# Kernel optimization log

Hardware: AMD Instinct MI355X
Metric: run time of the kernel (lower is better)

Reference implementation:

```python
import jax, jax.numpy as jnp
import numpy as np

B, T, D, H = 2, 2048, 1024, 16  # batch, seq, n_embed, n_head


def setup_inputs() -> dict:
    key = jax.random.key(0)
    ks = jax.random.split(key, 5)
    scale = 1.0 / np.sqrt(D)
    return {
        "x": jax.random.normal(ks[0], (B, T, D), dtype=jnp.float32),
        "Wq": jax.random.normal(ks[1], (D, D), dtype=jnp.float32) * scale,
        "Wk": jax.random.normal(ks[2], (D, D), dtype=jnp.float32) * scale,
        "Wv": jax.random.normal(ks[3], (D, D), dtype=jnp.float32) * scale,
        "Wo": jax.random.normal(ks[4], (D, D), dtype=jnp.float32) * scale,
    }


def reference(x, Wq, Wk, Wv, Wo):
    b, t, d = x.shape
    hd = d // H  # head_dim
    # projections -> [B, H, T, hd]
    q = (x @ Wq).reshape(b, t, H, hd).transpose(0, 2, 1, 3)
    k = (x @ Wk).reshape(b, t, H, hd).transpose(0, 2, 1, 3)
    v = (x @ Wv).reshape(b, t, H, hd).transpose(0, 2, 1, 3)
    # scaled scores [B, H, T, T] with causal mask
    e = jnp.einsum("bhqd,bhkd->bhqk", q, k) * (1.0 / np.sqrt(hd))
    causal = jnp.tril(jnp.ones((t, t), dtype=bool))
    e = jnp.where(causal[None, None], e, jnp.finfo(e.dtype).min)
    alpha = jax.nn.softmax(e, axis=-1)
    # attention output -> [B, T, D]
    attn = jnp.einsum("bhqk,bhkd->bhqd", alpha, v)
    attn = attn.transpose(0, 2, 1, 3).reshape(b, t, d)
    return attn @ Wo
```

## Files before the change

### kernel.cpp

```cpp
#include <hip/hip_runtime.h>
#include <hip/hip_bf16.h>
#include <math.h>


#define Bsz  2
#define Tseq 2048
#define Dm   1024
#define NH   16
#define HD   64

typedef short bf16x8 __attribute__((ext_vector_type(8)));
typedef float floatx4 __attribute__((ext_vector_type(4)));

__device__ __forceinline__ unsigned short f2bf(float f) {
    __hip_bfloat16 h = __float2bfloat16(f);
    return *reinterpret_cast<unsigned short*>(&h);
}

__device__ __forceinline__ unsigned short f2bf_fast(float f) {
    unsigned int u = __builtin_bit_cast(unsigned int, f);
    return (unsigned short)((u + 0x8000u) >> 16);
}

__device__ __forceinline__ void lds16(unsigned short* lds, const unsigned short* g) {
    __builtin_amdgcn_global_load_lds(
        (const __attribute__((address_space(1))) void*)g,
        (__attribute__((address_space(3))) void*)lds, 16, 0, 0);
}

__global__ __launch_bounds__(256) void cast_x(const float* __restrict__ x,
                                              unsigned short* __restrict__ xb) {
    const size_t i = (size_t)blockIdx.x * 256 + threadIdx.x;
    const float4 v = ((const float4*)x)[i];
    ushort4 o;
    o.x = f2bf(v.x); o.y = f2bf(v.y); o.z = f2bf(v.z); o.w = f2bf(v.w);
    ((ushort4*)xb)[i] = o;
}

__global__ __launch_bounds__(256) void wtrans(const float* __restrict__ W0,
                                              const float* __restrict__ W1,
                                              const float* __restrict__ W2,
                                              const float* __restrict__ W3,
                                              unsigned short* __restrict__ T0,
                                              unsigned short* __restrict__ T1,
                                              unsigned short* __restrict__ T2,
                                              unsigned short* __restrict__ T3) {
    const int z = blockIdx.z;
    const float* W = (z == 0) ? W0 : (z == 1) ? W1 : (z == 2) ? W2 : W3;
    unsigned short* T = (z == 0) ? T0 : (z == 1) ? T1 : (z == 2) ? T2 : T3;
    __shared__ float t[64][65];
    const int k0 = blockIdx.y * 64, n0 = blockIdx.x * 64;
    const int row = threadIdx.x >> 6, col = threadIdx.x & 63;
#pragma unroll
    for (int p = 0; p < 16; ++p)
        t[p * 4 + row][col] = W[(size_t)(k0 + p * 4 + row) * Dm + n0 + col];
    __syncthreads();
#pragma unroll
    for (int p = 0; p < 16; ++p)
        T[(size_t)(n0 + p * 4 + row) * Dm + k0 + col] = f2bf(t[col][p * 4 + row]);
}

__device__ __forceinline__ void gemm128_mainloop(const unsigned short* __restrict__ A,
                                                 const unsigned short* __restrict__ Bt,
                                                 int K, int m0, int n0,
                                                 unsigned short* As, unsigned short* Bs,
                                                 floatx4 acc[4][4]) {
    const int tid = threadIdx.x;
    const int lane = tid & 63, wave = tid >> 6;
    const int l15 = lane & 15, quad = lane >> 4;
    const int wm = (wave >> 1) * 64, wn = (wave & 1) * 64;

    for (int k0 = 0; k0 < K; k0 += 32) {
        __syncthreads();
#pragma unroll
        for (int c = 0; c < 2; ++c) {
            const int idx = c * 256 + tid;
            const int row = idx >> 2, kc = (idx & 3) * 8;
            lds16(&As[row * 32 + kc], A + (size_t)(m0 + row) * K + k0 + kc);
            lds16(&Bs[row * 32 + kc], Bt + (size_t)(n0 + row) * K + k0 + kc);
        }
        __syncthreads();
        bf16x8 af[4], bf[4];
#pragma unroll
        for (int i = 0; i < 4; ++i)
            af[i] = *(const bf16x8*)&As[(wm + i * 16 + l15) * 32 + quad * 8];
#pragma unroll
        for (int j = 0; j < 4; ++j)
            bf[j] = *(const bf16x8*)&Bs[(wn + j * 16 + l15) * 32 + quad * 8];
#pragma unroll
        for (int i = 0; i < 4; ++i)
#pragma unroll
            for (int j = 0; j < 4; ++j)
                acc[i][j] = __builtin_amdgcn_mfma_f32_16x16x32_bf16(af[i], bf[j], acc[i][j], 0, 0, 0);
    }
}

__global__ __launch_bounds__(256) void gemm_qkv(const unsigned short* __restrict__ xb,
                                                const unsigned short* __restrict__ Wqt,
                                                const unsigned short* __restrict__ Wkt,
                                                const unsigned short* __restrict__ Wvt,
                                                unsigned short* __restrict__ Qb,
                                                unsigned short* __restrict__ Kb,
                                                unsigned short* __restrict__ Vb) {
    __shared__ unsigned short As[128 * 32];
    __shared__ unsigned short Bs[128 * 32];
    const int z = blockIdx.z;
    const unsigned short* Bt = (z == 0) ? Wqt : (z == 1) ? Wkt : Wvt;
    unsigned short* C = (z == 0) ? Qb : (z == 1) ? Kb : Vb;
    const float scale = (z == 0) ? (0.125f * 1.4426950408889634f) : 1.0f;
    const int m0 = blockIdx.y * 128, n0 = blockIdx.x * 128;

    floatx4 acc[4][4];
#pragma unroll
    for (int i = 0; i < 4; ++i)
#pragma unroll
        for (int j = 0; j < 4; ++j) acc[i][j] = (floatx4){0.f, 0.f, 0.f, 0.f};

    gemm128_mainloop(xb, Bt, Dm, m0, n0, As, Bs, acc);

    const int lane = threadIdx.x & 63, wave = threadIdx.x >> 6;
    const int l15 = lane & 15, quad = lane >> 4;
    const int wm = (wave >> 1) * 64, wn = (wave & 1) * 64;
#pragma unroll
    for (int i = 0; i < 4; ++i)
#pragma unroll
        for (int j = 0; j < 4; ++j)
#pragma unroll
            for (int r = 0; r < 4; ++r) {
                const int row = m0 + wm + i * 16 + quad * 4 + r;
                const int col = n0 + wn + j * 16 + l15;
                C[(size_t)row * Dm + col] = f2bf(acc[i][j][r] * scale);
            }
}

__global__ __launch_bounds__(256) void gemm_out(const unsigned short* __restrict__ Yb,
                                                const unsigned short* __restrict__ Wot,
                                                float* __restrict__ out) {
    __shared__ unsigned short As[128 * 32];
    __shared__ unsigned short Bs[128 * 32];
    const int m0 = blockIdx.y * 128, n0 = blockIdx.x * 128;

    floatx4 acc[4][4];
#pragma unroll
    for (int i = 0; i < 4; ++i)
#pragma unroll
        for (int j = 0; j < 4; ++j) acc[i][j] = (floatx4){0.f, 0.f, 0.f, 0.f};

    gemm128_mainloop(Yb, Wot, Dm, m0, n0, As, Bs, acc);

    const int lane = threadIdx.x & 63, wave = threadIdx.x >> 6;
    const int l15 = lane & 15, quad = lane >> 4;
    const int wm = (wave >> 1) * 64, wn = (wave & 1) * 64;
#pragma unroll
    for (int i = 0; i < 4; ++i)
#pragma unroll
        for (int j = 0; j < 4; ++j)
#pragma unroll
            for (int r = 0; r < 4; ++r) {
                const int row = m0 + wm + i * 16 + quad * 4 + r;
                const int col = n0 + wn + j * 16 + l15;
                out[(size_t)row * Dm + col] = acc[i][j][r];
            }
}

__global__ __launch_bounds__(256) void vtrans_b(const unsigned short* __restrict__ Vb,
                                                unsigned short* __restrict__ VbT) {
    __shared__ unsigned short tile[64][72];
    const int tt = blockIdx.x;
    const int h = blockIdx.y;
    const int row = threadIdx.x >> 6, col = threadIdx.x & 63;
#pragma unroll
    for (int p = 0; p < 16; ++p)
        tile[p * 4 + row][col] = Vb[(size_t)(tt * 64 + p * 4 + row) * Dm + h * HD + col];
    __syncthreads();
    const int gt0 = tt * 64;
    const int b = gt0 / Tseq;
    const int lt0 = gt0 - b * Tseq;
#pragma unroll
    for (int p = 0; p < 16; ++p) {
        const int d = p * 4 + row;
        VbT[((size_t)(b * NH + h) * HD + d) * Tseq + lt0 + col] = tile[col][d];
    }
}

__global__ __launch_bounds__(256) void attn_mfma(const unsigned short* __restrict__ Qb,
                                                 const unsigned short* __restrict__ Kb,
                                                 const unsigned short* __restrict__ VbT,
                                                 unsigned short* __restrict__ Yb) {
    const int bh = blockIdx.x;
    const int b = bh >> 4;
    const int h = bh & 15;
    const int qt = 31 - blockIdx.y;
    const int tid = threadIdx.x;
    const int wave = tid >> 6;
    const int lane = tid & 63;
    const int l15 = lane & 15;
    const int quad = lane >> 4;

    __shared__ unsigned short Ks0[64][32];
    __shared__ unsigned short Ks1[64][32];
    __shared__ unsigned short Vt0[64][32];
    __shared__ unsigned short Vt1[64][32];
    __shared__ unsigned short Ps[4][16][72];

    const size_t tok0 = (size_t)b * Tseq;
    const int colh = h * HD;
    const unsigned short* vbase = VbT + (size_t)bh * HD * Tseq;

    const int qrow = qt * 64 + wave * 16;

    const unsigned short* qptr = Qb + (tok0 + qrow + l15) * Dm + colh + quad * 8;
    const bf16x8 qf0 = *(const bf16x8*)(qptr);
    const bf16x8 qf1 = *(const bf16x8*)(qptr + 32);

    float l_lane[4] = {0.f, 0.f, 0.f, 0.f};
    floatx4 o_acc[4];
#pragma unroll
    for (int t = 0; t < 4; ++t) o_acc[t] = (floatx4){0.f, 0.f, 0.f, 0.f};

    const int srow = tid >> 2;
    const int sc8 = (tid & 3) * 8;

    for (int kt = 0; kt <= qt; ++kt) {
        const int k0 = kt * 64;
        __syncthreads();
        {
            const unsigned short* krow = Kb + (tok0 + k0 + srow) * Dm + colh;
            const unsigned short* vrow = vbase + (size_t)srow * Tseq + k0;
            lds16(&Ks0[srow][sc8], krow + sc8);
            lds16(&Ks1[srow][sc8], krow + 32 + sc8);
            lds16(&Vt0[srow][sc8], vrow + sc8);
            lds16(&Vt1[srow][sc8], vrow + 32 + sc8);
        }
        __syncthreads();

        floatx4 s[4];
#pragma unroll
        for (int t = 0; t < 4; ++t) {
            floatx4 c = (floatx4){0.f, 0.f, 0.f, 0.f};
            const bf16x8 b0 = *(const bf16x8*)&Ks0[t * 16 + l15][quad * 8];
            const bf16x8 b1 = *(const bf16x8*)&Ks1[t * 16 + l15][quad * 8];
            c = __builtin_amdgcn_mfma_f32_16x16x32_bf16(qf0, b0, c, 0, 0, 0);
            c = __builtin_amdgcn_mfma_f32_16x16x32_bf16(qf1, b1, c, 0, 0, 0);
            s[t] = c;
        }

        if (kt == qt) {
#pragma unroll
            for (int t = 0; t < 4; ++t)
#pragma unroll
                for (int r = 0; r < 4; ++r) {
                    const int kl = t * 16 + l15;
                    const int ql = wave * 16 + quad * 4 + r;
                    if (kl > ql) s[t][r] = -1.0e30f;
                }
        }

#pragma unroll
        for (int t = 0; t < 4; ++t)
#pragma unroll
            for (int r = 0; r < 4; ++r) {
                const float p = __builtin_amdgcn_exp2f(s[t][r]);
                l_lane[r] += p;
                Ps[wave][quad * 4 + r][t * 16 + l15] = f2bf_fast(p);
            }

        const bf16x8 pa0 = *(const bf16x8*)&Ps[wave][l15][quad * 8];
        const bf16x8 pa1 = *(const bf16x8*)&Ps[wave][l15][32 + quad * 8];
#pragma unroll
        for (int t = 0; t < 4; ++t) {
            const bf16x8 vb0 = *(const bf16x8*)&Vt0[t * 16 + l15][quad * 8];
            const bf16x8 vb1 = *(const bf16x8*)&Vt1[t * 16 + l15][quad * 8];
            o_acc[t] = __builtin_amdgcn_mfma_f32_16x16x32_bf16(pa0, vb0, o_acc[t], 0, 0, 0);
            o_acc[t] = __builtin_amdgcn_mfma_f32_16x16x32_bf16(pa1, vb1, o_acc[t], 0, 0, 0);
        }
    }

#pragma unroll
    for (int off = 1; off < 16; off <<= 1)
#pragma unroll
        for (int r = 0; r < 4; ++r)
            l_lane[r] += __shfl_xor(l_lane[r], off);
    float inv_l[4];
#pragma unroll
    for (int r = 0; r < 4; ++r) inv_l[r] = 1.0f / l_lane[r];
#pragma unroll
    for (int t = 0; t < 4; ++t)
#pragma unroll
        for (int r = 0; r < 4; ++r) {
            const int q = qrow + quad * 4 + r;
            Yb[(tok0 + q) * Dm + colh + t * 16 + l15] = f2bf(o_acc[t][r] * inv_l[r]);
        }
}

extern "C" void kernel_launch(void* const* d_in, const int* in_sizes, int n_in,
                              void* d_out, int out_size, void* d_ws, size_t ws_size,
                              hipStream_t stream) {
    const float* x  = (const float*)d_in[0];
    const float* Wq = (const float*)d_in[1];
    const float* Wk = (const float*)d_in[2];
    const float* Wv = (const float*)d_in[3];
    const float* Wo = (const float*)d_in[4];
    float* out = (float*)d_out;

    const int M = Bsz * Tseq;
    char* ws = (char*)d_ws;
    unsigned short* xb  = (unsigned short*)(ws);
    unsigned short* Wqt = (unsigned short*)(ws + (((size_t)8)  << 20));
    unsigned short* Wkt = (unsigned short*)(ws + (((size_t)10) << 20));
    unsigned short* Wvt = (unsigned short*)(ws + (((size_t)12) << 20));
    unsigned short* Wot = (unsigned short*)(ws + (((size_t)14) << 20));
    unsigned short* Qb  = (unsigned short*)(ws + (((size_t)16) << 20));
    unsigned short* Kb  = (unsigned short*)(ws + (((size_t)24) << 20));
    unsigned short* Vb  = (unsigned short*)(ws + (((size_t)32) << 20));
    unsigned short* VbT = (unsigned short*)(ws + (((size_t)40) << 20));
    unsigned short* Yb  = (unsigned short*)(ws + (((size_t)48) << 20));

    dim3 blk(256);
    hipLaunchKernelGGL(cast_x, dim3((M * Dm) / (4 * 256)), blk, 0, stream, x, xb);
    hipLaunchKernelGGL(wtrans, dim3(16, 16, 4), blk, 0, stream,
                       Wq, Wk, Wv, Wo, Wqt, Wkt, Wvt, Wot);

    hipLaunchKernelGGL(gemm_qkv, dim3(Dm / 128, M / 128, 3), blk, 0, stream,
                       xb, Wqt, Wkt, Wvt, Qb, Kb, Vb);

    hipLaunchKernelGGL(vtrans_b, dim3(M / 64, NH), blk, 0, stream, Vb, VbT);

    hipLaunchKernelGGL(attn_mfma, dim3(Bsz * NH, 32), blk, 0, stream, Qb, Kb, VbT, Yb);

    hipLaunchKernelGGL(gemm_out, dim3(Dm / 128, M / 128), blk, 0, stream, Yb, Wot, out);
}
```

Baseline: 186.8 us.

## Use 128-row query tiles in attention and merge prep kernels into one launch

The attention kernel now gives each block 128 query rows, with each wave owning 32 rows as two 16-row MFMA sub-tiles. Every K/V tile loaded into LDS is therefore reused across twice as many queries, and the K/V fragments are read from LDS once per wave for both sub-tiles. Waves whose rows are entirely before a key tile skip its compute but still join the shared loads. Separately, the x bf16 cast and the weight transpose are merged into one kernel to save a launch. The trade-off is half as many attention blocks, more registers per wave, and more causal load imbalance across waves within a block.

Result: slower. 193.7 us (+3.7%).

```diff
diff --git a/kernel.cpp b/kernel.cpp
--- a/kernel.cpp
+++ b/kernel.cpp
@@ -28,27 +28,29 @@
         (__attribute__((address_space(3))) void*)lds, 16, 0, 0);
 }
 
-__global__ __launch_bounds__(256) void cast_x(const float* __restrict__ x,
-                                              unsigned short* __restrict__ xb) {
-    const size_t i = (size_t)blockIdx.x * 256 + threadIdx.x;
-    const float4 v = ((const float4*)x)[i];
-    ushort4 o;
-    o.x = f2bf(v.x); o.y = f2bf(v.y); o.z = f2bf(v.z); o.w = f2bf(v.w);
-    ((ushort4*)xb)[i] = o;
-}
-
-__global__ __launch_bounds__(256) void wtrans(const float* __restrict__ W0,
-                                              const float* __restrict__ W1,
-                                              const float* __restrict__ W2,
-                                              const float* __restrict__ W3,
-                                              unsigned short* __restrict__ T0,
-                                              unsigned short* __restrict__ T1,
-                                              unsigned short* __restrict__ T2,
-                                              unsigned short* __restrict__ T3) {
+__global__ __launch_bounds__(256) void prep(const float* __restrict__ x,
+                                            const float* __restrict__ W0,
+                                            const float* __restrict__ W1,
+                                            const float* __restrict__ W2,
+                                            const float* __restrict__ W3,
+                                            unsigned short* __restrict__ xb,
+                                            unsigned short* __restrict__ T0,
+                                            unsigned short* __restrict__ T1,
+                                            unsigned short* __restrict__ T2,
+                                            unsigned short* __restrict__ T3) {
+    __shared__ float t[64][65];
     const int z = blockIdx.z;
+    if (z >= 4) {
+        const int bi = (z - 4) * 256 + blockIdx.y * 16 + blockIdx.x;
+        const size_t i = (size_t)bi * 256 + threadIdx.x;
+        const float4 v = ((const float4*)x)[i];
+        ushort4 o;
+        o.x = f2bf(v.x); o.y = f2bf(v.y); o.z = f2bf(v.z); o.w = f2bf(v.w);
+        ((ushort4*)xb)[i] = o;
+        return;
+    }
     const float* W = (z == 0) ? W0 : (z == 1) ? W1 : (z == 2) ? W2 : W3;
     unsigned short* T = (z == 0) ? T0 : (z == 1) ? T1 : (z == 2) ? T2 : T3;
-    __shared__ float t[64][65];
     const int k0 = blockIdx.y * 64, n0 = blockIdx.x * 64;
     const int row = threadIdx.x >> 6, col = threadIdx.x & 63;
 #pragma unroll
@@ -190,7 +192,7 @@
     const int bh = blockIdx.x;
     const int b = bh >> 4;
     const int h = bh & 15;
-    const int qt = 31 - blockIdx.y;
+    const int qt128 = 15 - blockIdx.y;
     const int tid = threadIdx.x;
     const int wave = tid >> 6;
     const int lane = tid & 63;
@@ -201,27 +203,35 @@
     __shared__ unsigned short Ks1[64][32];
     __shared__ unsigned short Vt0[64][32];
     __shared__ unsigned short Vt1[64][32];
-    __shared__ unsigned short Ps[4][16][72];
+    __shared__ unsigned short Ps[4][32][72];
 
     const size_t tok0 = (size_t)b * Tseq;
     const int colh = h * HD;
     const unsigned short* vbase = VbT + (size_t)bh * HD * Tseq;
 
-    const int qrow = qt * 64 + wave * 16;
-
-    const unsigned short* qptr = Qb + (tok0 + qrow + l15) * Dm + colh + quad * 8;
-    const bf16x8 qf0 = *(const bf16x8*)(qptr);
-    const bf16x8 qf1 = *(const bf16x8*)(qptr + 32);
-
-    float l_lane[4] = {0.f, 0.f, 0.f, 0.f};
-    floatx4 o_acc[4];
-#pragma unroll
-    for (int t = 0; t < 4; ++t) o_acc[t] = (floatx4){0.f, 0.f, 0.f, 0.f};
+    const int qrow = qt128 * 128 + wave * 32;
+
+    bf16x8 qf[2][2];
+#pragma unroll
+    for (int qh = 0; qh < 2; ++qh) {
+        const unsigned short* qptr =
+            Qb + (tok0 + qrow + qh * 16 + l15) * Dm + colh + quad * 8;
+        qf[qh][0] = *(const bf16x8*)(qptr);
+        qf[qh][1] = *(const bf16x8*)(qptr + 32);
+    }
+
+    float l_lane[2][4] = {};
+    floatx4 o_acc[2][4];
+#pragma unroll
+    for (int qh = 0; qh < 2; ++qh)
+#pragma unroll
+        for (int t = 0; t < 4; ++t) o_acc[qh][t] = (floatx4){0.f, 0.f, 0.f, 0.f};
 
     const int srow = tid >> 2;
     const int sc8 = (tid & 3) * 8;
 
-    for (int kt = 0; kt <= qt; ++kt) {
+    const int nkt = 2 * qt128 + 2;
+    for (int kt = 0; kt < nkt; ++kt) {
         const int k0 = kt * 64;
         __syncthreads();
         {
@@ -233,64 +243,91 @@
             lds16(&Vt1[srow][sc8], vrow + 32 + sc8);
         }
         __syncthreads();
-
-        floatx4 s[4];
+        if (k0 > qrow + 31) continue;
+
+        bf16x8 kb0[4], kb1[4];
 #pragma unroll
         for (int t = 0; t < 4; ++t) {
-            floatx4 c = (floatx4){0.f, 0.f, 0.f, 0.f};
-            const bf16x8 b0 = *(const bf16x8*)&Ks0[t * 16 + l15][quad * 8];
-            const bf16x8 b1 = *(const bf16x8*)&Ks1[t * 16 + l15][quad * 8];
-            c = __builtin_amdgcn_mfma_f32_16x16x32_bf16(qf0, b0, c, 0, 0, 0);
-            c = __builtin_amdgcn_mfma_f32_16x16x32_bf16(qf1, b1, c, 0, 0, 0);
-            s[t] = c;
-        }
-
-        if (kt == qt) {
+            kb0[t] = *(const bf16x8*)&Ks0[t * 16 + l15][quad * 8];
+            kb1[t] = *(const bf16x8*)&Ks1[t * 16 + l15][quad * 8];
+        }
+
+        floatx4 s[2][4];
+#pragma unroll
+        for (int qh = 0; qh < 2; ++qh)
+#pragma unroll
+            for (int t = 0; t < 4; ++t) {
+                floatx4 c = (floatx4){0.f, 0.f, 0.f, 0.f};
+                c = __builtin_amdgcn_mfma_f32_16x16x32_bf16(qf[qh][0], kb0[t], c, 0, 0, 0);
+                c = __builtin_amdgcn_mfma_f32_16x16x32_bf16(qf[qh][1], kb1[t], c, 0, 0, 0);
+                s[qh][t] = c;
+            }
+
+        if (k0 + 63 > qrow) {
+#pragma unroll
+            for (int qh = 0; qh < 2; ++qh)
+#pragma unroll
+                for (int t = 0; t < 4; ++t)
+#pragma unroll
+                    for (int r = 0; r < 4; ++r) {
+                        const int kl = k0 + t * 16 + l15;
+                        const int ql = qrow + qh * 16 + quad * 4 + r;
+                        if (kl > ql) s[qh][t][r] = -1.0e30f;
+                    }
+        }
+
+#pragma unroll
+        for (int qh = 0; qh < 2; ++qh)
 #pragma unroll
             for (int t = 0; t < 4; ++t)
 #pragma unroll
                 for (int r = 0; r < 4; ++r) {
-                    const int kl = t * 16 + l15;
-                    const int ql = wave * 16 + quad * 4 + r;
-                    if (kl > ql) s[t][r] = -1.0e30f;
+                    const float p = __builtin_amdgcn_exp2f(s[qh][t][r]);
+                    l_lane[qh][r] += p;
+                    Ps[wave][qh * 16 + quad * 4 + r][t * 16 + l15] = f2bf_fast(p);
                 }
-        }
-
+
+        bf16x8 vb0[4], vb1[4];
+#pragma unroll
+        for (int t = 0; t < 4; ++t) {
+            vb0[t] = *(const bf16x8*)&Vt0[t * 16 + l15][quad * 8];
+            vb1[t] = *(const bf16x8*)&Vt1[t * 16 + l15][quad * 8];
+        }
+
+#pragma unroll
+        for (int qh = 0; qh < 2; ++qh) {
+            const bf16x8 pa0 = *(const bf16x8*)&Ps[wave][qh * 16 + l15][quad * 8];
+            const bf16x8 pa1 = *(const bf16x8*)&Ps[wave][qh * 16 + l15][32 + quad * 8];
+#pragma unroll
+            for (int t = 0; t < 4; ++t) {
+                o_acc[qh][t] = __builtin_amdgcn_mfma_f32_16x16x32_bf16(pa0, vb0[t], o_acc[qh][t], 0, 0, 0);
+                o_acc[qh][t] = __builtin_amdgcn_mfma_f32_16x16x32_bf16(pa1, vb1[t], o_acc[qh][t], 0, 0, 0);
+            }
+        }
+    }
+
+#pragma unroll
+    for (int off = 1; off < 16; off <<= 1)
+#pragma unroll
+        for (int qh = 0; qh < 2; ++qh)
+#pragma unroll
+            for (int r = 0; r < 4; ++r)
+                l_lane[qh][r] += __shfl_xor(l_lane[qh][r], off);
+    float inv_l[2][4];
+#pragma unroll
+    for (int qh = 0; qh < 2; ++qh)
+#pragma unroll
+        for (int r = 0; r < 4; ++r) inv_l[qh][r] = 1.0f / l_lane[qh][r];
+#pragma unroll
+    for (int qh = 0; qh < 2; ++qh)
 #pragma unroll
         for (int t = 0; t < 4; ++t)
 #pragma unroll
             for (int r = 0; r < 4; ++r) {
-                const float p = __builtin_amdgcn_exp2f(s[t][r]);
-                l_lane[r] += p;
-                Ps[wave][quad * 4 + r][t * 16 + l15] = f2bf_fast(p);
-            }
-
-        const bf16x8 pa0 = *(const bf16x8*)&Ps[wave][l15][quad * 8];
-        const bf16x8 pa1 = *(const bf16x8*)&Ps[wave][l15][32 + quad * 8];
-#pragma unroll
-        for (int t = 0; t < 4; ++t) {
-            const bf16x8 vb0 = *(const bf16x8*)&Vt0[t * 16 + l15][quad * 8];
-            const bf16x8 vb1 = *(const bf16x8*)&Vt1[t * 16 + l15][quad * 8];
-            o_acc[t] = __builtin_amdgcn_mfma_f32_16x16x32_bf16(pa0, vb0, o_acc[t], 0, 0, 0);
-            o_acc[t] = __builtin_amdgcn_mfma_f32_16x16x32_bf16(pa1, vb1, o_acc[t], 0, 0, 0);
-        }
-    }
-
-#pragma unroll
-    for (int off = 1; off < 16; off <<= 1)
-#pragma unroll
-        for (int r = 0; r < 4; ++r)
-            l_lane[r] += __shfl_xor(l_lane[r], off);
-    float inv_l[4];
-#pragma unroll
-    for (int r = 0; r < 4; ++r) inv_l[r] = 1.0f / l_lane[r];
-#pragma unroll
-    for (int t = 0; t < 4; ++t)
-#pragma unroll
-        for (int r = 0; r < 4; ++r) {
-            const int q = qrow + quad * 4 + r;
-            Yb[(tok0 + q) * Dm + colh + t * 16 + l15] = f2bf(o_acc[t][r] * inv_l[r]);
-        }
+                const int q = qrow + qh * 16 + quad * 4 + r;
+                Yb[(tok0 + q) * Dm + colh + t * 16 + l15] =
+                    f2bf(o_acc[qh][t][r] * inv_l[qh][r]);
+            }
 }
 
 extern "C" void kernel_launch(void* const* d_in, const int* in_sizes, int n_in,
@@ -317,16 +354,15 @@
     unsigned short* Yb  = (unsigned short*)(ws + (((size_t)48) << 20));
 
     dim3 blk(256);
-    hipLaunchKernelGGL(cast_x, dim3((M * Dm) / (4 * 256)), blk, 0, stream, x, xb);
-    hipLaunchKernelGGL(wtrans, dim3(16, 16, 4), blk, 0, stream,
-                       Wq, Wk, Wv, Wo, Wqt, Wkt, Wvt, Wot);
+    hipLaunchKernelGGL(prep, dim3(16, 16, 20), blk, 0, stream,
+                       x, Wq, Wk, Wv, Wo, xb, Wqt, Wkt, Wvt, Wot);
 
     hipLaunchKernelGGL(gemm_qkv, dim3(Dm / 128, M / 128, 3), blk, 0, stream,
                        xb, Wqt, Wkt, Wvt, Qb, Kb, Vb);
 
     hipLaunchKernelGGL(vtrans_b, dim3(M / 64, NH), blk, 0, stream, Vb, VbT);
 
-    hipLaunchKernelGGL(attn_mfma, dim3(Bsz * NH, 32), blk, 0, stream, Qb, Kb, VbT, Yb);
+    hipLaunchKernelGGL(attn_mfma, dim3(Bsz * NH, 16), blk, 0, stream, Qb, Kb, VbT, Yb);
 
     hipLaunchKernelGGL(gemm_out, dim3(Dm / 128, M / 128), blk, 0, stream, Yb, Wot, out);
 }
```

## Fuse prep kernels, write transposed V from QKV GEMM, shrink output GEMM tile

Applied to the files above, without the earlier changes.

Merges the x cast and weight transpose into one prep launch. The QKV GEMM now writes V straight into the per-head transposed layout, which removes the separate vtrans kernel and its round trip through global memory. The output GEMM moves to 128x64 tiles, doubling the block count to fill more CUs, but each block reuses less data. The transposed V stores are 8-byte, strided writes, so they coalesce less well than the old row stores.

After: 177.2 us. -5.2%, faster.

```diff
diff --git a/kernel.cpp b/kernel.cpp
--- a/kernel.cpp
+++ b/kernel.cpp
@@ -28,27 +28,29 @@
         (__attribute__((address_space(3))) void*)lds, 16, 0, 0);
 }
 
-__global__ __launch_bounds__(256) void cast_x(const float* __restrict__ x,
-                                              unsigned short* __restrict__ xb) {
-    const size_t i = (size_t)blockIdx.x * 256 + threadIdx.x;
-    const float4 v = ((const float4*)x)[i];
-    ushort4 o;
-    o.x = f2bf(v.x); o.y = f2bf(v.y); o.z = f2bf(v.z); o.w = f2bf(v.w);
-    ((ushort4*)xb)[i] = o;
-}
-
-__global__ __launch_bounds__(256) void wtrans(const float* __restrict__ W0,
-                                              const float* __restrict__ W1,
-                                              const float* __restrict__ W2,
-                                              const float* __restrict__ W3,
-                                              unsigned short* __restrict__ T0,
-                                              unsigned short* __restrict__ T1,
-                                              unsigned short* __restrict__ T2,
-                                              unsigned short* __restrict__ T3) {
+__global__ __launch_bounds__(256) void prep(const float* __restrict__ x,
+                                            const float* __restrict__ W0,
+                                            const float* __restrict__ W1,
+                                            const float* __restrict__ W2,
+                                            const float* __restrict__ W3,
+                                            unsigned short* __restrict__ xb,
+                                            unsigned short* __restrict__ T0,
+                                            unsigned short* __restrict__ T1,
+                                            unsigned short* __restrict__ T2,
+                                            unsigned short* __restrict__ T3) {
+    __shared__ float t[64][65];
     const int z = blockIdx.z;
+    if (z >= 4) {
+        const int bi = (z - 4) * 256 + blockIdx.y * 16 + blockIdx.x;
+        const size_t i = (size_t)bi * 256 + threadIdx.x;
+        const float4 v = ((const float4*)x)[i];
+        ushort4 o;
+        o.x = f2bf(v.x); o.y = f2bf(v.y); o.z = f2bf(v.z); o.w = f2bf(v.w);
+        ((ushort4*)xb)[i] = o;
+        return;
+    }
     const float* W = (z == 0) ? W0 : (z == 1) ? W1 : (z == 2) ? W2 : W3;
     unsigned short* T = (z == 0) ? T0 : (z == 1) ? T1 : (z == 2) ? T2 : T3;
-    __shared__ float t[64][65];
     const int k0 = blockIdx.y * 64, n0 = blockIdx.x * 64;
     const int row = threadIdx.x >> 6, col = threadIdx.x & 63;
 #pragma unroll
@@ -101,12 +103,11 @@
                                                 const unsigned short* __restrict__ Wvt,
                                                 unsigned short* __restrict__ Qb,
                                                 unsigned short* __restrict__ Kb,
-                                                unsigned short* __restrict__ Vb) {
+                                                unsigned short* __restrict__ VbT) {
     __shared__ unsigned short As[128 * 32];
     __shared__ unsigned short Bs[128 * 32];
     const int z = blockIdx.z;
     const unsigned short* Bt = (z == 0) ? Wqt : (z == 1) ? Wkt : Wvt;
-    unsigned short* C = (z == 0) ? Qb : (z == 1) ? Kb : Vb;
     const float scale = (z == 0) ? (0.125f * 1.4426950408889634f) : 1.0f;
     const int m0 = blockIdx.y * 128, n0 = blockIdx.x * 128;
 
@@ -121,6 +122,24 @@
     const int lane = threadIdx.x & 63, wave = threadIdx.x >> 6;
     const int l15 = lane & 15, quad = lane >> 4;
     const int wm = (wave >> 1) * 64, wn = (wave & 1) * 64;
+
+    if (z == 2) {
+#pragma unroll
+        for (int i = 0; i < 4; ++i)
+#pragma unroll
+            for (int j = 0; j < 4; ++j) {
+                const int col = n0 + wn + j * 16 + l15;
+                const int hh = col >> 6, dd = col & 63;
+                const int tok = m0 + wm + i * 16 + quad * 4;
+                const int bb = tok >> 11, tl = tok & (Tseq - 1);
+                ushort4 o;
+                o.x = f2bf(acc[i][j][0]); o.y = f2bf(acc[i][j][1]);
+                o.z = f2bf(acc[i][j][2]); o.w = f2bf(acc[i][j][3]);
+                *(ushort4*)&VbT[((size_t)((bb * NH + hh) * HD + dd)) * Tseq + tl] = o;
+            }
+        return;
+    }
+    unsigned short* C = (z == 0) ? Qb : Kb;
 #pragma unroll
     for (int i = 0; i < 4; ++i)
 #pragma unroll
@@ -137,50 +156,56 @@
                                                 const unsigned short* __restrict__ Wot,
                                                 float* __restrict__ out) {
     __shared__ unsigned short As[128 * 32];
-    __shared__ unsigned short Bs[128 * 32];
-    const int m0 = blockIdx.y * 128, n0 = blockIdx.x * 128;
-
-    floatx4 acc[4][4];
+    __shared__ unsigned short Bs[64 * 32];
+    const int m0 = blockIdx.y * 128, n0 = blockIdx.x * 64;
+    const int tid = threadIdx.x;
+    const int lane = tid & 63, wave = tid >> 6;
+    const int l15 = lane & 15, quad = lane >> 4;
+    const int wm = (wave >> 1) * 64, wn = (wave & 1) * 32;
+
+    floatx4 acc[4][2];
 #pragma unroll
     for (int i = 0; i < 4; ++i)
 #pragma unroll
-        for (int j = 0; j < 4; ++j) acc[i][j] = (floatx4){0.f, 0.f, 0.f, 0.f};
-
-    gemm128_mainloop(Yb, Wot, Dm, m0, n0, As, Bs, acc);
-
-    const int lane = threadIdx.x & 63, wave = threadIdx.x >> 6;
-    const int l15 = lane & 15, quad = lane >> 4;
-    const int wm = (wave >> 1) * 64, wn = (wave & 1) * 64;
+        for (int j = 0; j < 2; ++j) acc[i][j] = (floatx4){0.f, 0.f, 0.f, 0.f};
+
+    for (int k0 = 0; k0 < Dm; k0 += 32) {
+        __syncthreads();
+        {
+#pragma unroll
+            for (int c = 0; c < 2; ++c) {
+                const int idx = c * 256 + tid;
+                const int row = idx >> 2, kc = (idx & 3) * 8;
+                lds16(&As[row * 32 + kc], Yb + (size_t)(m0 + row) * Dm + k0 + kc);
+            }
+            const int row = tid >> 2, kc = (tid & 3) * 8;
+            lds16(&Bs[row * 32 + kc], Wot + (size_t)(n0 + row) * Dm + k0 + kc);
+        }
+        __syncthreads();
+        bf16x8 af[4], bf[2];
+#pragma unroll
+        for (int i = 0; i < 4; ++i)
+            af[i] = *(const bf16x8*)&As[(wm + i * 16 + l15) * 32 + quad * 8];
+#pragma unroll
+        for (int j = 0; j < 2; ++j)
+            bf[j] = *(const bf16x8*)&Bs[(wn + j * 16 + l15) * 32 + quad * 8];
+#pragma unroll
+        for (int i = 0; i < 4; ++i)
+#pragma unroll
+            for (int j = 0; j < 2; ++j)
+                acc[i][j] = __builtin_amdgcn_mfma_f32_16x16x32_bf16(af[i], bf[j], acc[i][j], 0, 0, 0);
+    }
+
 #pragma unroll
     for (int i = 0; i < 4; ++i)
 #pragma unroll
-        for (int j = 0; j < 4; ++j)
+        for (int j = 0; j < 2; ++j)
 #pragma unroll
             for (int r = 0; r < 4; ++r) {
                 const int row = m0 + wm + i * 16 + quad * 4 + r;
                 const int col = n0 + wn + j * 16 + l15;
                 out[(size_t)row * Dm + col] = acc[i][j][r];
             }
-}
-
-__global__ __launch_bounds__(256) void vtrans_b(const unsigned short* __restrict__ Vb,
-                                                unsigned short* __restrict__ VbT) {
-    __shared__ unsigned short tile[64][72];
-    const int tt = blockIdx.x;
-    const int h = blockIdx.y;
-    const int row = threadIdx.x >> 6, col = threadIdx.x & 63;
-#pragma unroll
-    for (int p = 0; p < 16; ++p)
-        tile[p * 4 + row][col] = Vb[(size_t)(tt * 64 + p * 4 + row) * Dm + h * HD + col];
-    __syncthreads();
-    const int gt0 = tt * 64;
-    const int b = gt0 / Tseq;
-    const int lt0 = gt0 - b * Tseq;
-#pragma unroll
-    for (int p = 0; p < 16; ++p) {
-        const int d = p * 4 + row;
-        VbT[((size_t)(b * NH + h) * HD + d) * Tseq + lt0 + col] = tile[col][d];
-    }
 }
 
 __global__ __launch_bounds__(256) void attn_mfma(const unsigned short* __restrict__ Qb,
@@ -312,21 +337,17 @@
     unsigned short* Wot = (unsigned short*)(ws + (((size_t)14) << 20));
     unsigned short* Qb  = (unsigned short*)(ws + (((size_t)16) << 20));
     unsigned short* Kb  = (unsigned short*)(ws + (((size_t)24) << 20));
-    unsigned short* Vb  = (unsigned short*)(ws + (((size_t)32) << 20));
-    unsigned short* VbT = (unsigned short*)(ws + (((size_t)40) << 20));
-    unsigned short* Yb  = (unsigned short*)(ws + (((size_t)48) << 20));
+    unsigned short* VbT = (unsigned short*)(ws + (((size_t)32) << 20));
+    unsigned short* Yb  = (unsigned short*)(ws + (((size_t)40) << 20));
 
     dim3 blk(256);
-    hipLaunchKernelGGL(cast_x, dim3((M * Dm) / (4 * 256)), blk, 0, stream, x, xb);
-    hipLaunchKernelGGL(wtrans, dim3(16, 16, 4), blk, 0, stream,
-                       Wq, Wk, Wv, Wo, Wqt, Wkt, Wvt, Wot);
+    hipLaunchKernelGGL(prep, dim3(16, 16, 20), blk, 0, stream,
+                       x, Wq, Wk, Wv, Wo, xb, Wqt, Wkt, Wvt, Wot);
 
     hipLaunchKernelGGL(gemm_qkv, dim3(Dm / 128, M / 128, 3), blk, 0, stream,
-                       xb, Wqt, Wkt, Wvt, Qb, Kb, Vb);
-
-    hipLaunchKernelGGL(vtrans_b, dim3(M / 64, NH), blk, 0, stream, Vb, VbT);
+                       xb, Wqt, Wkt, Wvt, Qb, Kb, VbT);
 
     hipLaunchKernelGGL(attn_mfma, dim3(Bsz * NH, 32), blk, 0, stream, Qb, Kb, VbT, Yb);
 
-    hipLaunchKernelGGL(gemm_out, dim3(Dm / 128, M / 128), blk, 0, stream, Yb, Wot, out);
-}
+    hipLaunchKernelGGL(gemm_out, dim3(Dm / 64, M / 128), blk, 0, stream, Yb, Wot, out);
+}
```
